# Kernel optimization log

Measured on AMD Instinct MI355X. Metric: run time of the kernel, lower is better.

## Reference

```python
import jax, jax.numpy as jnp
import numpy as np

D_MODEL = 1024
NUM_HEADS = 16
D_K = D_MODEL // NUM_HEADS


def setup_inputs() -> dict:
    key = jax.random.key(0)
    ks = jax.random.split(key, 10)
    s = 1.0 / np.sqrt(D_MODEL)  # ~ torch Linear init scale
    inp = {
        "x": jax.random.normal(ks[0], (2, 2048, D_MODEL), dtype=jnp.float32),
        "Wq": jax.random.uniform(ks[1], (D_MODEL, D_MODEL), jnp.float32, -s, s),
        "bq": jax.random.uniform(ks[2], (D_MODEL,), jnp.float32, -s, s),
        "Wk": jax.random.uniform(ks[3], (D_MODEL, D_MODEL), jnp.float32, -s, s),
        "bk": jax.random.uniform(ks[4], (D_MODEL,), jnp.float32, -s, s),
        "Wv": jax.random.uniform(ks[5], (D_MODEL, D_MODEL), jnp.float32, -s, s),
        "bv": jax.random.uniform(ks[6], (D_MODEL,), jnp.float32, -s, s),
        "Wo": jax.random.uniform(ks[7], (D_MODEL, D_MODEL), jnp.float32, -s, s),
        "bo": jax.random.uniform(ks[8], (D_MODEL,), jnp.float32, -s, s),
        "ln_gamma": jnp.ones((D_MODEL,), jnp.float32),
        "ln_beta": jnp.zeros((D_MODEL,), jnp.float32),
    }
    return inp


def reference(x, Wq, bq, Wk, bk, Wv, bv, Wo, bo, ln_gamma, ln_beta):
    B, S, D = x.shape
    residual = x
    # LayerNorm (eps=1e-5 as torch default)
    mu = jnp.mean(x, axis=-1, keepdims=True)
    var = jnp.mean(jnp.square(x - mu), axis=-1, keepdims=True)
    xn = (x - mu) * jax.lax.rsqrt(var + 1e-5) * ln_gamma + ln_beta
    # QKV projections (torch Linear: y = x @ W^T + b) -> (B, H, S, d_k)
    def proj(W, b):
        return (xn @ W.T + b).reshape(B, S, NUM_HEADS, D_K).transpose(0, 2, 1, 3)
    Q, K, V = proj(Wq, bq), proj(Wk, bk), proj(Wv, bv)
    scores = jnp.einsum("bhqd,bhkd->bhqk", Q, K) / np.sqrt(D_K).astype(np.float32)
    attn = jax.nn.softmax(scores, axis=-1)  # (B, H, S, S); dropout is no-op (eval)
    context = jnp.einsum("bhqk,bhkd->bhqd", attn, V)
    context = context.transpose(0, 2, 1, 3).reshape(B, S, D)
    out = context @ Wo.T + bo
    return out + residual, attn.mean(axis=1)
```

## Files before the change

kernel.cpp:

```cpp
#include <hip/hip_runtime.h>
#include <stdint.h>
#include <stddef.h>

#define DEV static __device__ __forceinline__

typedef float f32x4 __attribute__((ext_vector_type(4)));
typedef float f32x16 __attribute__((ext_vector_type(16)));
typedef unsigned u32x4 __attribute__((ext_vector_type(4)));
typedef __bf16 bf16x8 __attribute__((ext_vector_type(8)));

DEV short f2bf(float f) {
  union { float f; unsigned u; } a; a.f = f;
  unsigned r = a.u + 0x7fffu + ((a.u >> 16) & 1u);
  return (short)(r >> 16);
}

DEV void gld_lds16(const void* g, void* lds) {
  __builtin_amdgcn_global_load_lds(
      (__attribute__((address_space(1))) void*)(void*)g,
      (__attribute__((address_space(3))) void*)lds, 16, 0, 0);
}

DEV f32x4 MFMA(bf16x8 a, bf16x8 b, f32x4 c) {
  return __builtin_amdgcn_mfma_f32_16x16x32_bf16(a, b, c, 0, 0, 0);
}
DEV f32x16 MFMA32(bf16x8 a, bf16x8 b, f32x16 c) {
  return __builtin_amdgcn_mfma_f32_32x32x16_bf16(a, b, c, 0, 0, 0);
}

DEV float ex2(float x) { return __builtin_amdgcn_exp2f(x); }

DEV unsigned cvtpk(float lo, float hi) {
  unsigned r;
  asm("v_cvt_pk_bf16_f32 %0, %1, %2" : "=v"(r) : "v"(lo), "v"(hi));
  return r;
}

DEV float xhalf_max(float v) {
  float a = v, b = v;
  asm volatile("v_permlane32_swap_b32 %0, %1" : "+v"(a), "+v"(b));
  return fmaxf(a, b);
}
DEV float xhalf_sum(float v) {
  float a = v, b = v;
  asm volatile("v_permlane32_swap_b32 %0, %1" : "+v"(a), "+v"(b));
  return a + b;
}

#define LOG2E 1.4426950408889634f


__global__ __launch_bounds__(256) void k_cvtw(const float* __restrict__ w0,
                                              const float* __restrict__ w1,
                                              const float* __restrict__ w2,
                                              const float* __restrict__ w3,
                                              short* __restrict__ dst) {
  int i = blockIdx.x * 256 + threadIdx.x;
  int sel = i >> 18;
  const float* src = sel == 0 ? w0 : sel == 1 ? w1 : sel == 2 ? w2 : w3;
  int off = (i & 0x3ffff) * 4;
  float4 v = *(const float4*)(src + off);
  short4 o4; o4.x = f2bf(v.x); o4.y = f2bf(v.y); o4.z = f2bf(v.z); o4.w = f2bf(v.w);
  *(short4*)(dst + (size_t)i * 4) = o4;
}

__global__ __launch_bounds__(256) void k_ln(const float* __restrict__ x,
                                            const float* __restrict__ g,
                                            const float* __restrict__ be,
                                            short* __restrict__ xn) {
  int row = blockIdx.x;
  int t = threadIdx.x;
  const float4* xr = (const float4*)(x + (size_t)row * 1024);
  float4 v = xr[t];
  float s = v.x + v.y + v.z + v.w;
  float ss = v.x * v.x + v.y * v.y + v.z * v.z + v.w * v.w;
#pragma unroll
  for (int o = 32; o; o >>= 1) { s += __shfl_down(s, o); ss += __shfl_down(ss, o); }
  __shared__ float ps[4], pss[4];
  int w = t >> 6, lane = t & 63;
  if (lane == 0) { ps[w] = s; pss[w] = ss; }
  __syncthreads();
  float st = ps[0] + ps[1] + ps[2] + ps[3];
  float sst = pss[0] + pss[1] + pss[2] + pss[3];
  float mean = st * (1.0f / 1024.0f);
  float var = sst * (1.0f / 1024.0f) - mean * mean;
  float rstd = rsqrtf(var + 1e-5f);
  float4 gv = ((const float4*)g)[t];
  float4 bv = ((const float4*)be)[t];
  short4 o4;
  o4.x = f2bf((v.x - mean) * rstd * gv.x + bv.x);
  o4.y = f2bf((v.y - mean) * rstd * gv.y + bv.y);
  o4.z = f2bf((v.z - mean) * rstd * gv.z + bv.z);
  o4.w = f2bf((v.w - mean) * rstd * gv.w + bv.w);
  ((short4*)(xn + (size_t)row * 1024))[t] = o4;
}

__global__ __launch_bounds__(256) void k_gemm_qkv(
    const short* __restrict__ xn, const short* __restrict__ wbf,
    const float* __restrict__ bq, const float* __restrict__ bk,
    const float* __restrict__ bv, short* __restrict__ q_ws,
    short* __restrict__ k_ws, short* __restrict__ v_ws) {
  __shared__ __align__(16) short at[128 * 32];
  __shared__ __align__(16) short bt[128 * 32];
  int t = threadIdx.x, lane = t & 63, w = t >> 6;
  int wr = w >> 1, wc = w & 1;
  int z = blockIdx.z;
  int row0 = blockIdx.y * 128, col0 = blockIdx.x * 128;
  const short* A = xn + (size_t)row0 * 1024;
  const short* Bw = wbf + (size_t)z * (1024 * 1024) + (size_t)col0 * 1024;
  f32x4 acc[4][4];
#pragma unroll
  for (int m = 0; m < 4; m++)
#pragma unroll
    for (int n = 0; n < 4; n++) acc[m][n] = (f32x4)0.0f;

  for (int k0 = 0; k0 < 1024; k0 += 32) {
#pragma unroll
    for (int i = 0; i < 2; i++) {
      int c = t + i * 256;
      int r = c >> 2, cc = (c & 3) * 8;
      gld_lds16(A + (size_t)r * 1024 + k0 + cc, &at[c * 8]);
      gld_lds16(Bw + (size_t)r * 1024 + k0 + cc, &bt[c * 8]);
    }
    __syncthreads();
    bf16x8 af[4], bfr[4];
#pragma unroll
    for (int m = 0; m < 4; m++)
      af[m] = *(const bf16x8*)&at[(wr * 64 + m * 16 + (lane & 15)) * 32 + (lane >> 4) * 8];
#pragma unroll
    for (int n = 0; n < 4; n++)
      bfr[n] = *(const bf16x8*)&bt[(wc * 64 + n * 16 + (lane & 15)) * 32 + (lane >> 4) * 8];
#pragma unroll
    for (int m = 0; m < 4; m++)
#pragma unroll
      for (int n = 0; n < 4; n++) acc[m][n] = MFMA(af[m], bfr[n], acc[m][n]);
    __syncthreads();
  }
  const float* bias = z == 0 ? bq : z == 1 ? bk : bv;
  short* dst = z == 0 ? q_ws : z == 1 ? k_ws : v_ws;
  float scal = z == 0 ? (0.125f * LOG2E) : 1.0f;
#pragma unroll
  for (int m = 0; m < 4; m++)
#pragma unroll
    for (int n = 0; n < 4; n++)
#pragma unroll
      for (int r = 0; r < 4; r++) {
        int grow = row0 + wr * 64 + m * 16 + (lane >> 4) * 4 + r;
        int gcol = col0 + wc * 64 + n * 16 + (lane & 15);
        float val = (acc[m][n][r] + bias[gcol]) * scal;
        int bb = grow >> 11, s = grow & 2047, h = gcol >> 6, d = gcol & 63;
        dst[(((size_t)bb * 16 + h) * 2048 + s) * 64 + d] = f2bf(val);
      }
}

__global__ __launch_bounds__(256) void k_trv(const short* __restrict__ v_ws,
                                             short* __restrict__ vt_ws) {
  __shared__ short tile[64][65];
  int bh = blockIdx.y, s0 = blockIdx.x * 64;
  const short* src = v_ws + ((size_t)bh * 2048 + s0) * 64;
  int t = threadIdx.x;
#pragma unroll
  for (int i = 0; i < 4; i++) {
    int c = t + i * 256;
    int r = c >> 4, d4 = (c & 15) * 4;
    short4 v4 = *(const short4*)&src[r * 64 + d4];
    tile[d4 + 0][r] = v4.x; tile[d4 + 1][r] = v4.y;
    tile[d4 + 2][r] = v4.z; tile[d4 + 3][r] = v4.w;
  }
  __syncthreads();
#pragma unroll
  for (int i = 0; i < 4; i++) {
    int c = t + i * 256;
    int d = c >> 4, r4 = (c & 15) * 4;
    short4 o4;
    o4.x = tile[d][r4 + 0]; o4.y = tile[d][r4 + 1];
    o4.z = tile[d][r4 + 2]; o4.w = tile[d][r4 + 3];
    *(short4*)&vt_ws[((size_t)bh * 64 + d) * 2048 + s0 + r4] = o4;
  }
}

__global__ __launch_bounds__(256) void k_attn1(
    const short* __restrict__ q_ws, const short* __restrict__ k_ws,
    const short* __restrict__ vt_ws, short* __restrict__ o_ws,
    float* __restrict__ m_ws, float* __restrict__ l_ws) {
  __shared__ __align__(16) short k_lds[2][64 * 64];
  __shared__ __align__(16) short vt_lds[2][64 * 64];
  int t = threadIdx.x, lane = t & 63, w = t >> 6;
  int hi = lane >> 5, l31 = lane & 31;
  int qt = blockIdx.x, hd = blockIdx.y, b = blockIdx.z;
  int bh = b * 16 + hd;
  int q0 = qt * 128;
  const short* qb = q_ws + (size_t)bh * (2048 * 64);
  const short* kb = k_ws + (size_t)bh * (2048 * 64);
  const short* vtb = vt_ws + (size_t)bh * (64 * 2048);
  int qg = q0 + w * 32 + l31;

  bf16x8 qf[4];
#pragma unroll
  for (int d4 = 0; d4 < 4; d4++)
    qf[d4] = *(const bf16x8*)&qb[(size_t)qg * 64 + d4 * 16 + hi * 8];
  asm volatile("s_waitcnt vmcnt(0)" ::: "memory");

  const short *kp0, *kp1, *vp0, *vp1;
  {
    int c = t, r = c >> 3, j = (c & 7) ^ (r & 7);
    kp0 = kb + (size_t)r * 64 + j * 8;
    vp0 = vtb + (size_t)r * 2048 + j * 8;
  }
  {
    int c = t + 256, r = c >> 3, j = (c & 7) ^ (r & 7);
    kp1 = kb + (size_t)r * 64 + j * 8;
    vp1 = vtb + (size_t)r * 2048 + j * 8;
  }

#define STG_K(kt_, buf)                                     \
  {                                                         \
    gld_lds16(kp0 + (kt_) * 4096, &k_lds[buf][t * 8]);      \
    gld_lds16(kp1 + (kt_) * 4096, &k_lds[buf][(t + 256) * 8]); \
  }
#define STG_V(kt_, buf)                                     \
  {                                                         \
    gld_lds16(vp0 + (kt_) * 64, &vt_lds[buf][t * 8]);       \
    gld_lds16(vp1 + (kt_) * 64, &vt_lds[buf][(t + 256) * 8]); \
  }

  STG_K(0, 0);

  f32x16 Oacc[2];
#pragma unroll
  for (int i = 0; i < 16; i++) { Oacc[0][i] = 0.0f; Oacc[1][i] = 0.0f; }
  float mrun = -1e30f, lrun = 0.0f;
  bf16x8 pb0, pb1, pb2, pb3;

  for (int it = 0; it < 32; ++it) {
    STG_V(it, it & 1);
    STG_K(it < 31 ? it + 1 : 31, (it + 1) & 1);
    asm volatile("s_waitcnt vmcnt(4)" ::: "memory");
    __builtin_amdgcn_s_barrier();

    const short* kl = k_lds[it & 1];
    const short* vl = vt_lds[(it ^ 1) & 1];

    __builtin_amdgcn_s_setprio(1);
    f32x16 S0 = (f32x16)0.0f, S1 = (f32x16)0.0f;
#pragma unroll
    for (int d4 = 0; d4 < 4; d4++) {
      int row0 = l31;
      bf16x8 kf0 = *(const bf16x8*)&kl[row0 * 64 + (((d4 * 2 + hi) ^ (row0 & 7)) * 8)];
      int row1 = 32 + l31;
      bf16x8 kf1 = *(const bf16x8*)&kl[row1 * 64 + (((d4 * 2 + hi) ^ (row1 & 7)) * 8)];
      S0 = MFMA32(kf0, qf[d4], S0);
      S1 = MFMA32(kf1, qf[d4], S1);
    }
    if (it) {
#pragma unroll
      for (int ks = 0; ks < 4; ks++) {
        bf16x8 pk = ks == 0 ? pb0 : ks == 1 ? pb1 : ks == 2 ? pb2 : pb3;
        int row0 = l31;
        bf16x8 vf0 = *(const bf16x8*)&vl[row0 * 64 + (((ks * 2 + hi) ^ (row0 & 7)) * 8)];
        int row1 = 32 + l31;
        bf16x8 vf1 = *(const bf16x8*)&vl[row1 * 64 + (((ks * 2 + hi) ^ (row1 & 7)) * 8)];
        Oacc[0] = MFMA32(vf0, pk, Oacc[0]);
        Oacc[1] = MFMA32(vf1, pk, Oacc[1]);
      }
    }
    __builtin_amdgcn_s_setprio(0);

    float mt;
    {
      float a[8];
#pragma unroll
      for (int i = 0; i < 8; i++)
        a[i] = fmaxf(fmaxf(S0[i], S0[i + 8]), fmaxf(S1[i], S1[i + 8]));
      float b0 = fmaxf(fmaxf(a[0], a[1]), fmaxf(a[2], a[3]));
      float b1 = fmaxf(fmaxf(a[4], a[5]), fmaxf(a[6], a[7]));
      mt = xhalf_max(fmaxf(b0, b1));
    }
    if (!__all(mt - mrun <= 8.0f)) {
      float mn = fmaxf(mrun, mt);
      float sc_ = ex2(mrun - mn);
      lrun *= sc_;
#pragma unroll
      for (int i = 0; i < 16; i++) { Oacc[0][i] *= sc_; Oacc[1][i] *= sc_; }
      mrun = mn;
    }
    float rs0 = 0.0f, rs1 = 0.0f;
#pragma unroll
    for (int i = 0; i < 16; i++) {
      float p0 = ex2(S0[i] - mrun);
      float p1 = ex2(S1[i] - mrun);
      S0[i] = p0; S1[i] = p1;
      rs0 += p0; rs1 += p1;
    }
    lrun += xhalf_sum(rs0 + rs1);

    {
      unsigned wA, wB, wC, wD;
      wA = cvtpk(S0[0], S0[1]);  wB = cvtpk(S0[2], S0[3]);
      wC = cvtpk(S0[4], S0[5]);  wD = cvtpk(S0[6], S0[7]);
      asm volatile("v_permlane32_swap_b32 %0, %1" : "+v"(wA), "+v"(wC));
      asm volatile("v_permlane32_swap_b32 %0, %1" : "+v"(wB), "+v"(wD));
      u32x4 uu; uu.x = wA; uu.y = wB; uu.z = wC; uu.w = wD;
      pb0 = __builtin_bit_cast(bf16x8, uu);
      wA = cvtpk(S0[8], S0[9]);  wB = cvtpk(S0[10], S0[11]);
      wC = cvtpk(S0[12], S0[13]); wD = cvtpk(S0[14], S0[15]);
      asm volatile("v_permlane32_swap_b32 %0, %1" : "+v"(wA), "+v"(wC));
      asm volatile("v_permlane32_swap_b32 %0, %1" : "+v"(wB), "+v"(wD));
      uu.x = wA; uu.y = wB; uu.z = wC; uu.w = wD;
      pb1 = __builtin_bit_cast(bf16x8, uu);
      wA = cvtpk(S1[0], S1[1]);  wB = cvtpk(S1[2], S1[3]);
      wC = cvtpk(S1[4], S1[5]);  wD = cvtpk(S1[6], S1[7]);
      asm volatile("v_permlane32_swap_b32 %0, %1" : "+v"(wA), "+v"(wC));
      asm volatile("v_permlane32_swap_b32 %0, %1" : "+v"(wB), "+v"(wD));
      uu.x = wA; uu.y = wB; uu.z = wC; uu.w = wD;
      pb2 = __builtin_bit_cast(bf16x8, uu);
      wA = cvtpk(S1[8], S1[9]);  wB = cvtpk(S1[10], S1[11]);
      wC = cvtpk(S1[12], S1[13]); wD = cvtpk(S1[14], S1[15]);
      asm volatile("v_permlane32_swap_b32 %0, %1" : "+v"(wA), "+v"(wC));
      asm volatile("v_permlane32_swap_b32 %0, %1" : "+v"(wB), "+v"(wD));
      uu.x = wA; uu.y = wB; uu.z = wC; uu.w = wD;
      pb3 = __builtin_bit_cast(bf16x8, uu);
    }
    __builtin_amdgcn_s_barrier();
  }
  asm volatile("s_waitcnt vmcnt(0)" ::: "memory");
  __builtin_amdgcn_s_barrier();

  {
    const short* vl = vt_lds[1];
    __builtin_amdgcn_s_setprio(1);
#pragma unroll
    for (int ks = 0; ks < 4; ks++) {
      bf16x8 pk = ks == 0 ? pb0 : ks == 1 ? pb1 : ks == 2 ? pb2 : pb3;
      int row0 = l31;
      bf16x8 vf0 = *(const bf16x8*)&vl[row0 * 64 + (((ks * 2 + hi) ^ (row0 & 7)) * 8)];
      int row1 = 32 + l31;
      bf16x8 vf1 = *(const bf16x8*)&vl[row1 * 64 + (((ks * 2 + hi) ^ (row1 & 7)) * 8)];
      Oacc[0] = MFMA32(vf0, pk, Oacc[0]);
      Oacc[1] = MFMA32(vf1, pk, Oacc[1]);
    }
    __builtin_amdgcn_s_setprio(0);
  }

  float rl = 1.0f / lrun;
  if (lane < 32) {
    m_ws[bh * 2048 + qg] = mrun;
    l_ws[bh * 2048 + qg] = rl;
  }
#pragma unroll
  for (int dt = 0; dt < 2; dt++)
#pragma unroll
    for (int g = 0; g < 4; g++) {
      short4 o4;
      o4.x = f2bf(Oacc[dt][g * 4 + 0] * rl);
      o4.y = f2bf(Oacc[dt][g * 4 + 1] * rl);
      o4.z = f2bf(Oacc[dt][g * 4 + 2] * rl);
      o4.w = f2bf(Oacc[dt][g * 4 + 3] * rl);
      int d = dt * 32 + g * 8 + hi * 4;
      *(short4*)&o_ws[((size_t)(b * 2048 + qg)) * 1024 + hd * 64 + d] = o4;
    }
}

__global__ __launch_bounds__(256, 3) void k_attn2(
    const short* __restrict__ q_ws, const short* __restrict__ k_ws,
    const float* __restrict__ m_ws, const float* __restrict__ l_ws,
    float* __restrict__ out1) {
  __shared__ __align__(16) short q_lds[2][64 * 64];
  __shared__ __align__(16) short k_lds2[2][128 * 64];
  __shared__ __align__(16) float ml_lds[2][2][64];
  int t = threadIdx.x, lane = t & 63, w = t >> 6;
  int k2 = blockIdx.x * 128, q0 = blockIdx.y * 64, b = blockIdx.z;

  f32x4 pacc[8];
#pragma unroll
  for (int n = 0; n < 8; n++) pacc[n] = (f32x4)0.0f;

#define STAGE2(hh, buf)                                                          \
  {                                                                              \
    int bh_ = b * 16 + (hh);                                                     \
    const short* qb_ = q_ws + (size_t)bh_ * (2048 * 64);                         \
    const short* kb_ = k_ws + (size_t)bh_ * (2048 * 64);                         \
    _Pragma("unroll")                                                            \
    for (int i = 0; i < 2; i++) {                                                \
      int c = t + i * 256;                                                       \
      int r = c >> 3, j = (c & 7) ^ (r & 7);                                     \
      gld_lds16(qb_ + (size_t)(q0 + r) * 64 + j * 8, &q_lds[buf][c * 8]);        \
    }                                                                            \
    _Pragma("unroll")                                                            \
    for (int i = 0; i < 4; i++) {                                                \
      int c = t + i * 256;                                                       \
      int r = c >> 3, j = (c & 7) ^ (r & 7);                                     \
      gld_lds16(kb_ + (size_t)(k2 + r) * 64 + j * 8, &k_lds2[buf][c * 8]);       \
    }                                                                            \
    int cc = w * 8 + (t & 63);                                                   \
    if ((t & 63) < 8) {                                                          \
      const float* src_ = cc < 16 ? &m_ws[(size_t)bh_ * 2048 + q0 + cc * 4]      \
                                  : &l_ws[(size_t)bh_ * 2048 + q0 + (cc - 16) * 4]; \
      gld_lds16(src_, &ml_lds[buf][0][cc * 4]);                                  \
    }                                                                            \
  }

  STAGE2(0, 0);
  int cur = 0;
  for (int h = 0; h < 16; ++h) {
    int hn = h < 15 ? h + 1 : 15;
    STAGE2(hn, cur ^ 1);
    asm volatile("s_waitcnt vmcnt(7)" ::: "memory");
    __builtin_amdgcn_s_barrier();

    const short* ql = q_lds[cur];
    const short* kl = k_lds2[cur];
    bf16x8 qf[2];
#pragma unroll
    for (int kf = 0; kf < 2; kf++) {
      int row = w * 16 + (lane & 15);
      qf[kf] = *(const bf16x8*)&ql[row * 64 + (((kf * 4 + (lane >> 4)) ^ (row & 7)) * 8)];
    }
    f32x4 sc[8];
#pragma unroll
    for (int n = 0; n < 8; n++) sc[n] = (f32x4)0.0f;
#pragma unroll
    for (int kf = 0; kf < 2; kf++)
#pragma unroll
      for (int n = 0; n < 8; n++) {
        int row = n * 16 + (lane & 15);
        bf16x8 kfr = *(const bf16x8*)&kl[row * 64 + (((kf * 4 + (lane >> 4)) ^ (row & 7)) * 8)];
        sc[n] = MFMA(qf[kf], kfr, sc[n]);
      }
    f32x4 mh = *(const f32x4*)&ml_lds[cur][0][w * 16 + (lane >> 4) * 4];
    f32x4 lh = *(const f32x4*)&ml_lds[cur][1][w * 16 + (lane >> 4) * 4];
#pragma unroll
    for (int n = 0; n < 8; n++)
#pragma unroll
      for (int r = 0; r < 4; r++)
        pacc[n][r] += ex2(sc[n][r] - mh[r]) * lh[r];
    __builtin_amdgcn_s_barrier();
    cur ^= 1;
  }

#pragma unroll
  for (int n = 0; n < 8; n++)
#pragma unroll
    for (int r = 0; r < 4; r++) {
      int q = q0 + w * 16 + (lane >> 4) * 4 + r;
      int k = k2 + n * 16 + (lane & 15);
      out1[((size_t)b * 2048 + q) * 2048 + k] = pacc[n][r] * 0.0625f;
    }
}

__global__ __launch_bounds__(256) void k_gemm_out(
    const short* __restrict__ o_ws, const short* __restrict__ wo_bf,
    const float* __restrict__ bo, const float* __restrict__ x,
    float* __restrict__ out0) {
  __shared__ __align__(16) short at[128 * 32];
  __shared__ __align__(16) short bt[128 * 32];
  int t = threadIdx.x, lane = t & 63, w = t >> 6;
  int wr = w >> 1, wc = w & 1;
  int row0 = blockIdx.y * 128, col0 = blockIdx.x * 128;
  const short* A = o_ws + (size_t)row0 * 1024;
  const short* Bw = wo_bf + (size_t)col0 * 1024;
  f32x4 acc[4][4];
#pragma unroll
  for (int m = 0; m < 4; m++)
#pragma unroll
    for (int n = 0; n < 4; n++) acc[m][n] = (f32x4)0.0f;

  for (int k0 = 0; k0 < 1024; k0 += 32) {
#pragma unroll
    for (int i = 0; i < 2; i++) {
      int c = t + i * 256;
      int r = c >> 2, cc = (c & 3) * 8;
      gld_lds16(A + (size_t)r * 1024 + k0 + cc, &at[c * 8]);
      gld_lds16(Bw + (size_t)r * 1024 + k0 + cc, &bt[c * 8]);
    }
    __syncthreads();
    bf16x8 af[4], bfr[4];
#pragma unroll
    for (int m = 0; m < 4; m++)
      af[m] = *(const bf16x8*)&at[(wr * 64 + m * 16 + (lane & 15)) * 32 + (lane >> 4) * 8];
#pragma unroll
    for (int n = 0; n < 4; n++)
      bfr[n] = *(const bf16x8*)&bt[(wc * 64 + n * 16 + (lane & 15)) * 32 + (lane >> 4) * 8];
#pragma unroll
    for (int m = 0; m < 4; m++)
#pragma unroll
      for (int n = 0; n < 4; n++) acc[m][n] = MFMA(af[m], bfr[n], acc[m][n]);
    __syncthreads();
  }
#pragma unroll
  for (int m = 0; m < 4; m++)
#pragma unroll
    for (int n = 0; n < 4; n++)
#pragma unroll
      for (int r = 0; r < 4; r++) {
        int grow = row0 + wr * 64 + m * 16 + (lane >> 4) * 4 + r;
        int gcol = col0 + wc * 64 + n * 16 + (lane & 15);
        float val = acc[m][n][r] + bo[gcol] + x[(size_t)grow * 1024 + gcol];
        out0[(size_t)grow * 1024 + gcol] = val;
      }
}

extern "C" void kernel_launch(void* const* d_in, const int* in_sizes, int n_in,
                              void* d_out, int out_size, void* d_ws, size_t ws_size,
                              hipStream_t stream) {
  (void)in_sizes; (void)n_in; (void)out_size; (void)ws_size;
  const float* x   = (const float*)d_in[0];
  const float* Wq  = (const float*)d_in[1];
  const float* bq  = (const float*)d_in[2];
  const float* Wk  = (const float*)d_in[3];
  const float* bk  = (const float*)d_in[4];
  const float* Wv  = (const float*)d_in[5];
  const float* bv  = (const float*)d_in[6];
  const float* Wo  = (const float*)d_in[7];
  const float* bo  = (const float*)d_in[8];
  const float* lng = (const float*)d_in[9];
  const float* lnb = (const float*)d_in[10];
  float* out0 = (float*)d_out;
  float* out1 = out0 + (size_t)2 * 2048 * 1024;

  char* ws = (char*)d_ws;
  short* xn    = (short*)(ws);
  short* q_ws  = (short*)(ws + 8388608);
  short* k_ws  = (short*)(ws + 16777216);
  short* o_ws  = (short*)(ws + 25165824);
  short* vt_ws = (short*)(ws + 33554432);
  short* wbf   = (short*)(ws + 41943040);
  float* m_ws  = (float*)(ws + 50331648);
  float* l_ws  = (float*)(ws + 50593792);

  k_cvtw<<<4096, 256, 0, stream>>>(Wq, Wk, Wv, Wo, wbf);
  k_ln<<<4096, 256, 0, stream>>>(x, lng, lnb, xn);
  k_gemm_qkv<<<dim3(8, 32, 3), 256, 0, stream>>>(xn, wbf, bq, bk, bv, q_ws, k_ws, o_ws);
  k_trv<<<dim3(32, 32), 256, 0, stream>>>(o_ws, vt_ws);
  k_attn1<<<dim3(16, 16, 2), 256, 0, stream>>>(q_ws, k_ws, vt_ws, o_ws, m_ws, l_ws);
  k_attn2<<<dim3(16, 32, 2), 256, 0, stream>>>(q_ws, k_ws, m_ws, l_ws, out1);
  k_gemm_out<<<dim3(8, 32), 256, 0, stream>>>(o_ws, wbf + (size_t)3 * 1024 * 1024, bo, x, out0);
}
```

Measured before the change: 168.1 us.

## Fuse V transpose into QKV GEMM, widen GEMM K-tiles, remap blocks, enlarge attention blocks

Several changes at once. The QKV GEMM now writes V transposed through an LDS staging tile, which removes the separate transpose kernel. Both GEMMs move to a 64-wide K step with an XOR-swizzled LDS layout and a block-index remap meant to improve L2 reuse. LayerNorm now handles one row per wavefront with no block-level barrier, and attention blocks grow to 512 threads covering 256 queries each, with one staged load per thread and a paired-float row-sum. The trade-offs are more LDS per GEMM block and possible register pressure, plus occupancy changes from the larger attention blocks.

```diff
diff --git a/kernel.cpp b/kernel.cpp
--- a/kernel.cpp
+++ b/kernel.cpp
@@ -4,6 +4,7 @@
 
 #define DEV static __device__ __forceinline__
 
+typedef float f32x2 __attribute__((ext_vector_type(2)));
 typedef float f32x4 __attribute__((ext_vector_type(4)));
 typedef float f32x16 __attribute__((ext_vector_type(16)));
 typedef unsigned u32x4 __attribute__((ext_vector_type(4)));
@@ -68,44 +69,49 @@
                                             const float* __restrict__ g,
                                             const float* __restrict__ be,
                                             short* __restrict__ xn) {
-  int row = blockIdx.x;
-  int t = threadIdx.x;
+  int w = threadIdx.x >> 6, lane = threadIdx.x & 63;
+  int row = blockIdx.x * 4 + w;
   const float4* xr = (const float4*)(x + (size_t)row * 1024);
-  float4 v = xr[t];
-  float s = v.x + v.y + v.z + v.w;
-  float ss = v.x * v.x + v.y * v.y + v.z * v.z + v.w * v.w;
-#pragma unroll
-  for (int o = 32; o; o >>= 1) { s += __shfl_down(s, o); ss += __shfl_down(ss, o); }
-  __shared__ float ps[4], pss[4];
-  int w = t >> 6, lane = t & 63;
-  if (lane == 0) { ps[w] = s; pss[w] = ss; }
-  __syncthreads();
-  float st = ps[0] + ps[1] + ps[2] + ps[3];
-  float sst = pss[0] + pss[1] + pss[2] + pss[3];
-  float mean = st * (1.0f / 1024.0f);
-  float var = sst * (1.0f / 1024.0f) - mean * mean;
+  float4 v[4];
+  float s = 0.0f, ss = 0.0f;
+#pragma unroll
+  for (int i = 0; i < 4; i++) {
+    v[i] = xr[lane + i * 64];
+    s += v[i].x + v[i].y + v[i].z + v[i].w;
+    ss += v[i].x * v[i].x + v[i].y * v[i].y + v[i].z * v[i].z + v[i].w * v[i].w;
+  }
+#pragma unroll
+  for (int o = 32; o; o >>= 1) { s += __shfl_xor(s, o); ss += __shfl_xor(ss, o); }
+  float mean = s * (1.0f / 1024.0f);
+  float var = ss * (1.0f / 1024.0f) - mean * mean;
   float rstd = rsqrtf(var + 1e-5f);
-  float4 gv = ((const float4*)g)[t];
-  float4 bv = ((const float4*)be)[t];
-  short4 o4;
-  o4.x = f2bf((v.x - mean) * rstd * gv.x + bv.x);
-  o4.y = f2bf((v.y - mean) * rstd * gv.y + bv.y);
-  o4.z = f2bf((v.z - mean) * rstd * gv.z + bv.z);
-  o4.w = f2bf((v.w - mean) * rstd * gv.w + bv.w);
-  ((short4*)(xn + (size_t)row * 1024))[t] = o4;
+#pragma unroll
+  for (int i = 0; i < 4; i++) {
+    float4 gv = ((const float4*)g)[lane + i * 64];
+    float4 bv = ((const float4*)be)[lane + i * 64];
+    short4 o4;
+    o4.x = f2bf((v[i].x - mean) * rstd * gv.x + bv.x);
+    o4.y = f2bf((v[i].y - mean) * rstd * gv.y + bv.y);
+    o4.z = f2bf((v[i].z - mean) * rstd * gv.z + bv.z);
+    o4.w = f2bf((v[i].w - mean) * rstd * gv.w + bv.w);
+    ((short4*)(xn + (size_t)row * 1024))[lane + i * 64] = o4;
+  }
 }
 
 __global__ __launch_bounds__(256) void k_gemm_qkv(
     const short* __restrict__ xn, const short* __restrict__ wbf,
     const float* __restrict__ bq, const float* __restrict__ bk,
     const float* __restrict__ bv, short* __restrict__ q_ws,
-    short* __restrict__ k_ws, short* __restrict__ v_ws) {
-  __shared__ __align__(16) short at[128 * 32];
-  __shared__ __align__(16) short bt[128 * 32];
+    short* __restrict__ k_ws, short* __restrict__ vt_ws) {
+  __shared__ __align__(16) short lds[16384];
+  short* at = lds;
+  short* bt = lds + 8192;
   int t = threadIdx.x, lane = t & 63, w = t >> 6;
   int wr = w >> 1, wc = w & 1;
-  int z = blockIdx.z;
-  int row0 = blockIdx.y * 128, col0 = blockIdx.x * 128;
+  int flat = blockIdx.x + 8 * blockIdx.y + 256 * blockIdx.z;
+  int mm = (flat & 7) * 96 + (flat >> 3);
+  int z = mm >> 8;
+  int row0 = ((mm >> 3) & 31) * 128, col0 = (mm & 7) * 128;
   const short* A = xn + (size_t)row0 * 1024;
   const short* Bw = wbf + (size_t)z * (1024 * 1024) + (size_t)col0 * 1024;
   f32x4 acc[4][4];
@@ -114,72 +120,86 @@
 #pragma unroll
     for (int n = 0; n < 4; n++) acc[m][n] = (f32x4)0.0f;
 
-  for (int k0 = 0; k0 < 1024; k0 += 32) {
-#pragma unroll
-    for (int i = 0; i < 2; i++) {
+  for (int k0 = 0; k0 < 1024; k0 += 64) {
+#pragma unroll
+    for (int i = 0; i < 4; i++) {
       int c = t + i * 256;
-      int r = c >> 2, cc = (c & 3) * 8;
-      gld_lds16(A + (size_t)r * 1024 + k0 + cc, &at[c * 8]);
-      gld_lds16(Bw + (size_t)r * 1024 + k0 + cc, &bt[c * 8]);
+      int r = c >> 3, j = ((c & 7) ^ (r & 7)) * 8;
+      gld_lds16(A + (size_t)r * 1024 + k0 + j, &at[c * 8]);
+      gld_lds16(Bw + (size_t)r * 1024 + k0 + j, &bt[c * 8]);
     }
     __syncthreads();
-    bf16x8 af[4], bfr[4];
+#pragma unroll
+    for (int kk = 0; kk < 2; kk++) {
+      bf16x8 af[4], bfr[4];
+#pragma unroll
+      for (int m = 0; m < 4; m++) {
+        int row = wr * 64 + m * 16 + (lane & 15);
+        af[m] = *(const bf16x8*)&at[row * 64 + (((kk * 4 + (lane >> 4)) ^ (row & 7)) * 8)];
+      }
+#pragma unroll
+      for (int n = 0; n < 4; n++) {
+        int row = wc * 64 + n * 16 + (lane & 15);
+        bfr[n] = *(const bf16x8*)&bt[row * 64 + (((kk * 4 + (lane >> 4)) ^ (row & 7)) * 8)];
+      }
+#pragma unroll
+      for (int m = 0; m < 4; m++)
+#pragma unroll
+        for (int n = 0; n < 4; n++) acc[m][n] = MFMA(af[m], bfr[n], acc[m][n]);
+    }
+    __syncthreads();
+  }
+
+  if (z < 2) {
+    const float* bias = z == 0 ? bq : bk;
+    short* dst = z == 0 ? q_ws : k_ws;
+    float scal = z == 0 ? (0.125f * LOG2E) : 1.0f;
 #pragma unroll
     for (int m = 0; m < 4; m++)
-      af[m] = *(const bf16x8*)&at[(wr * 64 + m * 16 + (lane & 15)) * 32 + (lane >> 4) * 8];
-#pragma unroll
-    for (int n = 0; n < 4; n++)
-      bfr[n] = *(const bf16x8*)&bt[(wc * 64 + n * 16 + (lane & 15)) * 32 + (lane >> 4) * 8];
-#pragma unroll
-    for (int m = 0; m < 4; m++)
-#pragma unroll
-      for (int n = 0; n < 4; n++) acc[m][n] = MFMA(af[m], bfr[n], acc[m][n]);
-    __syncthreads();
-  }
-  const float* bias = z == 0 ? bq : z == 1 ? bk : bv;
-  short* dst = z == 0 ? q_ws : z == 1 ? k_ws : v_ws;
-  float scal = z == 0 ? (0.125f * LOG2E) : 1.0f;
-#pragma unroll
-  for (int m = 0; m < 4; m++)
-#pragma unroll
-    for (int n = 0; n < 4; n++)
-#pragma unroll
-      for (int r = 0; r < 4; r++) {
-        int grow = row0 + wr * 64 + m * 16 + (lane >> 4) * 4 + r;
-        int gcol = col0 + wc * 64 + n * 16 + (lane & 15);
-        float val = (acc[m][n][r] + bias[gcol]) * scal;
-        int bb = grow >> 11, s = grow & 2047, h = gcol >> 6, d = gcol & 63;
-        dst[(((size_t)bb * 16 + h) * 2048 + s) * 64 + d] = f2bf(val);
-      }
-}
-
-__global__ __launch_bounds__(256) void k_trv(const short* __restrict__ v_ws,
-                                             short* __restrict__ vt_ws) {
-  __shared__ short tile[64][65];
-  int bh = blockIdx.y, s0 = blockIdx.x * 64;
-  const short* src = v_ws + ((size_t)bh * 2048 + s0) * 64;
-  int t = threadIdx.x;
-#pragma unroll
-  for (int i = 0; i < 4; i++) {
-    int c = t + i * 256;
-    int r = c >> 4, d4 = (c & 15) * 4;
-    short4 v4 = *(const short4*)&src[r * 64 + d4];
-    tile[d4 + 0][r] = v4.x; tile[d4 + 1][r] = v4.y;
-    tile[d4 + 2][r] = v4.z; tile[d4 + 3][r] = v4.w;
-  }
-  __syncthreads();
-#pragma unroll
-  for (int i = 0; i < 4; i++) {
-    int c = t + i * 256;
-    int d = c >> 4, r4 = (c & 15) * 4;
-    short4 o4;
-    o4.x = tile[d][r4 + 0]; o4.y = tile[d][r4 + 1];
-    o4.z = tile[d][r4 + 2]; o4.w = tile[d][r4 + 3];
-    *(short4*)&vt_ws[((size_t)bh * 64 + d) * 2048 + s0 + r4] = o4;
-  }
-}
-
-__global__ __launch_bounds__(256) void k_attn1(
+#pragma unroll
+      for (int n = 0; n < 4; n++)
+#pragma unroll
+        for (int r = 0; r < 4; r++) {
+          int grow = row0 + wr * 64 + m * 16 + (lane >> 4) * 4 + r;
+          int gcol = col0 + wc * 64 + n * 16 + (lane & 15);
+          float val = (acc[m][n][r] + bias[gcol]) * scal;
+          int bb = grow >> 11, s = grow & 2047, h = gcol >> 6, d = gcol & 63;
+          dst[(((size_t)bb * 16 + h) * 2048 + s) * 64 + d] = f2bf(val);
+        }
+  } else {
+    short* tb = lds;
+    int b = row0 >> 11, s0 = row0 & 2047;
+#pragma unroll
+    for (int hblk = 0; hblk < 2; hblk++) {
+      __syncthreads();
+      if (wc == hblk) {
+#pragma unroll
+        for (int m = 0; m < 4; m++)
+#pragma unroll
+          for (int n = 0; n < 4; n++)
+#pragma unroll
+            for (int r = 0; r < 4; r++) {
+              int srow = wr * 64 + m * 16 + (lane >> 4) * 4 + r;
+              int d = n * 16 + (lane & 15);
+              int gcol = col0 + hblk * 64 + d;
+              tb[d * 136 + srow] = f2bf(acc[m][n][r] + bv[gcol]);
+            }
+      }
+      __syncthreads();
+      int head = (col0 >> 6) + hblk;
+      int bh = b * 16 + head;
+#pragma unroll
+      for (int i = 0; i < 4; i++) {
+        int c = t + i * 256;
+        int d = c >> 4, sc = (c & 15) * 8;
+        bf16x8 vv = *(const bf16x8*)&tb[d * 136 + sc];
+        *(bf16x8*)&vt_ws[((size_t)bh * 64 + d) * 2048 + s0 + sc] = vv;
+      }
+    }
+  }
+}
+
+__global__ __launch_bounds__(512) void k_attn1(
     const short* __restrict__ q_ws, const short* __restrict__ k_ws,
     const short* __restrict__ vt_ws, short* __restrict__ o_ws,
     float* __restrict__ m_ws, float* __restrict__ l_ws) {
@@ -187,9 +207,11 @@
   __shared__ __align__(16) short vt_lds[2][64 * 64];
   int t = threadIdx.x, lane = t & 63, w = t >> 6;
   int hi = lane >> 5, l31 = lane & 31;
-  int qt = blockIdx.x, hd = blockIdx.y, b = blockIdx.z;
+  int flat = blockIdx.x + 8 * (blockIdx.y + 16 * blockIdx.z);
+  int mm = (flat & 7) * 32 + (flat >> 3);
+  int qt = mm & 7, hd = (mm >> 3) & 15, b = mm >> 7;
   int bh = b * 16 + hd;
-  int q0 = qt * 128;
+  int q0 = qt * 256;
   const short* qb = q_ws + (size_t)bh * (2048 * 64);
   const short* kb = k_ws + (size_t)bh * (2048 * 64);
   const short* vtb = vt_ws + (size_t)bh * (64 * 2048);
@@ -201,28 +223,15 @@
     qf[d4] = *(const bf16x8*)&qb[(size_t)qg * 64 + d4 * 16 + hi * 8];
   asm volatile("s_waitcnt vmcnt(0)" ::: "memory");
 
-  const short *kp0, *kp1, *vp0, *vp1;
+  const short *kp0, *vp0;
   {
-    int c = t, r = c >> 3, j = (c & 7) ^ (r & 7);
+    int r = t >> 3, j = (t & 7) ^ (r & 7);
     kp0 = kb + (size_t)r * 64 + j * 8;
     vp0 = vtb + (size_t)r * 2048 + j * 8;
   }
-  {
-    int c = t + 256, r = c >> 3, j = (c & 7) ^ (r & 7);
-    kp1 = kb + (size_t)r * 64 + j * 8;
-    vp1 = vtb + (size_t)r * 2048 + j * 8;
-  }
-
-#define STG_K(kt_, buf)                                     \
-  {                                                         \
-    gld_lds16(kp0 + (kt_) * 4096, &k_lds[buf][t * 8]);      \
-    gld_lds16(kp1 + (kt_) * 4096, &k_lds[buf][(t + 256) * 8]); \
-  }
-#define STG_V(kt_, buf)                                     \
-  {                                                         \
-    gld_lds16(vp0 + (kt_) * 64, &vt_lds[buf][t * 8]);       \
-    gld_lds16(vp1 + (kt_) * 64, &vt_lds[buf][(t + 256) * 8]); \
-  }
+
+#define STG_K(kt_, buf) gld_lds16(kp0 + (size_t)(kt_) * 4096, &k_lds[buf][t * 8])
+#define STG_V(kt_, buf) gld_lds16(vp0 + (size_t)(kt_) * 64, &vt_lds[buf][t * 8])
 
   STG_K(0, 0);
 
@@ -235,7 +244,7 @@
   for (int it = 0; it < 32; ++it) {
     STG_V(it, it & 1);
     STG_K(it < 31 ? it + 1 : 31, (it + 1) & 1);
-    asm volatile("s_waitcnt vmcnt(4)" ::: "memory");
+    asm volatile("s_waitcnt vmcnt(2)" ::: "memory");
     __builtin_amdgcn_s_barrier();
 
     const short* kl = k_lds[it & 1];
@@ -284,15 +293,22 @@
       for (int i = 0; i < 16; i++) { Oacc[0][i] *= sc_; Oacc[1][i] *= sc_; }
       mrun = mn;
     }
-    float rs0 = 0.0f, rs1 = 0.0f;
 #pragma unroll
     for (int i = 0; i < 16; i++) {
-      float p0 = ex2(S0[i] - mrun);
-      float p1 = ex2(S1[i] - mrun);
-      S0[i] = p0; S1[i] = p1;
-      rs0 += p0; rs1 += p1;
-    }
-    lrun += xhalf_sum(rs0 + rs1);
+      S0[i] = ex2(S0[i] - mrun);
+      S1[i] = ex2(S1[i] - mrun);
+    }
+    {
+      f32x2 a2; a2.x = 0.0f; a2.y = 0.0f;
+#pragma unroll
+      for (int i = 0; i < 8; i++) {
+        f32x2 t0, t1;
+        t0.x = S0[2 * i]; t0.y = S0[2 * i + 1];
+        t1.x = S1[2 * i]; t1.y = S1[2 * i + 1];
+        a2 += t0 + t1;
+      }
+      lrun += xhalf_sum(a2.x + a2.y);
+    }
 
     {
       unsigned wA, wB, wC, wD;
@@ -452,11 +468,14 @@
     const short* __restrict__ o_ws, const short* __restrict__ wo_bf,
     const float* __restrict__ bo, const float* __restrict__ x,
     float* __restrict__ out0) {
-  __shared__ __align__(16) short at[128 * 32];
-  __shared__ __align__(16) short bt[128 * 32];
+  __shared__ __align__(16) short lds[16384];
+  short* at = lds;
+  short* bt = lds + 8192;
   int t = threadIdx.x, lane = t & 63, w = t >> 6;
   int wr = w >> 1, wc = w & 1;
-  int row0 = blockIdx.y * 128, col0 = blockIdx.x * 128;
+  int flat = blockIdx.x + 8 * blockIdx.y;
+  int mm = (flat & 7) * 32 + (flat >> 3);
+  int row0 = (mm >> 3) * 128, col0 = (mm & 7) * 128;
   const short* A = o_ws + (size_t)row0 * 1024;
   const short* Bw = wo_bf + (size_t)col0 * 1024;
   f32x4 acc[4][4];
@@ -465,26 +484,33 @@
 #pragma unroll
     for (int n = 0; n < 4; n++) acc[m][n] = (f32x4)0.0f;
 
-  for (int k0 = 0; k0 < 1024; k0 += 32) {
-#pragma unroll
-    for (int i = 0; i < 2; i++) {
+  for (int k0 = 0; k0 < 1024; k0 += 64) {
+#pragma unroll
+    for (int i = 0; i < 4; i++) {
       int c = t + i * 256;
-      int r = c >> 2, cc = (c & 3) * 8;
-      gld_lds16(A + (size_t)r * 1024 + k0 + cc, &at[c * 8]);
-      gld_lds16(Bw + (size_t)r * 1024 + k0 + cc, &bt[c * 8]);
+      int r = c >> 3, j = ((c & 7) ^ (r & 7)) * 8;
+      gld_lds16(A + (size_t)r * 1024 + k0 + j, &at[c * 8]);
+      gld_lds16(Bw + (size_t)r * 1024 + k0 + j, &bt[c * 8]);
     }
     __syncthreads();
-    bf16x8 af[4], bfr[4];
-#pragma unroll
-    for (int m = 0; m < 4; m++)
-      af[m] = *(const bf16x8*)&at[(wr * 64 + m * 16 + (lane & 15)) * 32 + (lane >> 4) * 8];
-#pragma unroll
-    for (int n = 0; n < 4; n++)
-      bfr[n] = *(const bf16x8*)&bt[(wc * 64 + n * 16 + (lane & 15)) * 32 + (lane >> 4) * 8];
-#pragma unroll
-    for (int m = 0; m < 4; m++)
-#pragma unroll
-      for (int n = 0; n < 4; n++) acc[m][n] = MFMA(af[m], bfr[n], acc[m][n]);
+#pragma unroll
+    for (int kk = 0; kk < 2; kk++) {
+      bf16x8 af[4], bfr[4];
+#pragma unroll
+      for (int m = 0; m < 4; m++) {
+        int row = wr * 64 + m * 16 + (lane & 15);
+        af[m] = *(const bf16x8*)&at[row * 64 + (((kk * 4 + (lane >> 4)) ^ (row & 7)) * 8)];
+      }
+#pragma unroll
+      for (int n = 0; n < 4; n++) {
+        int row = wc * 64 + n * 16 + (lane & 15);
+        bfr[n] = *(const bf16x8*)&bt[row * 64 + (((kk * 4 + (lane >> 4)) ^ (row & 7)) * 8)];
+      }
+#pragma unroll
+      for (int m = 0; m < 4; m++)
+#pragma unroll
+        for (int n = 0; n < 4; n++) acc[m][n] = MFMA(af[m], bfr[n], acc[m][n]);
+    }
     __syncthreads();
   }
 #pragma unroll
@@ -529,10 +555,9 @@
   float* l_ws  = (float*)(ws + 50593792);
 
   k_cvtw<<<4096, 256, 0, stream>>>(Wq, Wk, Wv, Wo, wbf);
-  k_ln<<<4096, 256, 0, stream>>>(x, lng, lnb, xn);
-  k_gemm_qkv<<<dim3(8, 32, 3), 256, 0, stream>>>(xn, wbf, bq, bk, bv, q_ws, k_ws, o_ws);
-  k_trv<<<dim3(32, 32), 256, 0, stream>>>(o_ws, vt_ws);
-  k_attn1<<<dim3(16, 16, 2), 256, 0, stream>>>(q_ws, k_ws, vt_ws, o_ws, m_ws, l_ws);
+  k_ln<<<1024, 256, 0, stream>>>(x, lng, lnb, xn);
+  k_gemm_qkv<<<dim3(8, 32, 3), 256, 0, stream>>>(xn, wbf, bq, bk, bv, q_ws, k_ws, vt_ws);
+  k_attn1<<<dim3(8, 16, 2), 512, 0, stream>>>(q_ws, k_ws, vt_ws, o_ws, m_ws, l_ws);
   k_attn2<<<dim3(16, 32, 2), 256, 0, stream>>>(q_ws, k_ws, m_ws, l_ws, out1);
   k_gemm_out<<<dim3(8, 32), 256, 0, stream>>>(o_ws, wbf + (size_t)3 * 1024 * 1024, bo, x, out0);
 }
```

Result: slower. 191.6 us (+14.0%).
